# Performance work log

Hardware: AMD Instinct MI355X
Metric: run time of the kernel (lower is better)

The kernel has to match this reference:

```python
import jax, jax.numpy as jnp
import numpy as np

N = 50000      # nodes
E = 800000     # edges (avg degree 16)
IN = 128       # in_dim
OUT = 128      # out_dim
K = 4          # Chebyshev order
NEIG = 64      # num_eigs
H = 128        # eigval_hidden_dim
BN_EPS = 1e-5


def setup_inputs() -> dict:
    key = jax.random.key(0)
    ks = jax.random.split(key, 12)
    feature = jax.random.normal(ks[0], (N, IN), jnp.float32)
    # linear over concat of (K Chebyshev blocks + 1 spectral block) = (K+1)*IN
    lin_w = jax.random.normal(ks[1], ((K + 1) * IN, OUT), jnp.float32) / np.sqrt((K + 1) * IN)
    lin_b = jnp.zeros((OUT,), jnp.float32)
    # eigval_filter MLP: 1 -> H -> H -> 1 (ReLU between)
    ew0 = jax.random.normal(ks[2], (1, H), jnp.float32)
    eb0 = jnp.zeros((H,), jnp.float32)
    ew1 = jax.random.normal(ks[3], (H, H), jnp.float32) / np.sqrt(H)
    eb1 = jnp.zeros((H,), jnp.float32)
    ew2 = jax.random.normal(ks[4], (H, 1), jnp.float32) / np.sqrt(H)
    eb2 = jnp.zeros((1,), jnp.float32)
    bn_gamma = jnp.ones((OUT,), jnp.float32)
    bn_beta = jnp.zeros((OUT,), jnp.float32)
    lambda_max = jnp.ones((1,), jnp.float32)
    # cached (detached) spectral data for the graph
    evecs = jax.random.normal(ks[5], (N, NEIG), jnp.float32)
    evals = jax.random.uniform(ks[6], (NEIG,), jnp.float32)
    edge_src = jax.random.randint(ks[7], (E,), 0, N, jnp.int32).astype(jnp.int64)
    edge_dst = jax.random.randint(ks[8], (E,), 0, N, jnp.int32).astype(jnp.int64)
    return dict(feature=feature, lin_w=lin_w, lin_b=lin_b, ew0=ew0, eb0=eb0,
                ew1=ew1, eb1=eb1, ew2=ew2, eb2=eb2, bn_gamma=bn_gamma,
                bn_beta=bn_beta, lambda_max=lambda_max, evecs=evecs,
                evals=evals, edge_src=edge_src, edge_dst=edge_dst)


def reference(feature, lin_w, lin_b, ew0, eb0, ew1, eb1, ew2, eb2,
              bn_gamma, bn_beta, lambda_max, evecs, evals, edge_src, edge_dst):
    src = edge_src.astype(jnp.int32)
    dst = edge_dst.astype(jnp.int32)
    # in-degrees (messages arrive at dst) and D^-1/2, clamped at 1
    deg = jax.ops.segment_sum(jnp.ones((E,), jnp.float32), dst, num_segments=N)
    d_sqrt = jnp.clip(deg, 1.0, None) ** -0.5  # [N]
    d_sqrt = d_sqrt[:, None]                   # [N,1]

    def unn_laplacian(x):
        m = (x * d_sqrt)[src]                              # [E,IN]
        agg = jax.ops.segment_sum(m, dst, num_segments=N)  # [N,IN]
        return agg * d_sqrt

    re_norm = 2.0 / lambda_max  # broadcast scalar (per-node in dgl, constant here)

    X0 = feature
    blocks = [X0]
    h = unn_laplacian(X0)
    X1 = -re_norm * h + X0 * (re_norm - 1.0)
    blocks.append(X1)
    for _ in range(2, K):
        h = unn_laplacian(X1)
        Xi = -2.0 * re_norm * h + X1 * 2.0 * (re_norm - 1.0) - X0
        blocks.append(Xi)
        X1, X0 = Xi, X1

    # spectral filtering: evecs^T f, scale by MLP(evals), project back
    z = jax.nn.relu(evals[:, None] @ ew0 + eb0)   # [NEIG,H]
    z = jax.nn.relu(z @ ew1 + eb1)                # [NEIG,H]
    ef = z @ ew2 + eb2                            # [NEIG,1]
    hs = jnp.einsum('ne,nf->ef', evecs, feature)  # [NEIG,IN]
    hs = ef * hs
    hs = jnp.einsum('ne,ef->nf', evecs, hs)       # [N,IN]
    blocks.append(hs)

    Xt = jnp.concatenate(blocks, axis=1)          # [N,(K+1)*IN]
    out = Xt @ lin_w + lin_b                      # [N,OUT]

    # BatchNorm1d (training-mode batch statistics, biased variance)
    mu = jnp.mean(out, axis=0)
    var = jnp.mean((out - mu) ** 2, axis=0)
    out = (out - mu) * jax.lax.rsqrt(var + BN_EPS) * bn_gamma + bn_beta
    out = jax.nn.relu(out)
    # dropout p=0.0 -> identity; residual disabled
    return out
```

## Files before the change

### kernel.cpp

```cpp
#include <hip/hip_runtime.h>

#define N_NODES 50000
#define N_EDGES 800000
#define IN_F    128
#define OUT_F   128
#define NEIG    64
#define HDIM    128
#define BN_EPSF 1e-5f
#define XB_ROWS 50048
#define XB_COLS 640
#define SCAN_BLK 49
#define HSP_BLOCKS 521
#define HSP_NODES 96
#define RED_CHUNK 33
#define RED_SPLIT 16

typedef __attribute__((ext_vector_type(8))) short short8;
typedef __attribute__((ext_vector_type(4))) float floatx4;

#define OFF_XB      0
#define OFF_X1F     (XB_ROWS * XB_COLS / 2)
#define OFF_X2F     (OFF_X1F + N_NODES * IN_F)
#define OFF_WT      (OFF_X2F + N_NODES * IN_F)
#define OFF_DSQRT   (OFF_WT + 40960)
#define OFF_HS      (OFF_DSQRT + N_NODES)
#define OFF_EF      (OFF_HS + NEIG * OUT_F)
#define OFF_COLSUM  (OFF_EF + NEIG)
#define OFF_COLSQ   (OFF_COLSUM + OUT_F)
#define OFF_DEG     (OFF_COLSQ + OUT_F)
#define OFF_ROWSTART (OFF_DEG + N_NODES)
#define OFF_CSR     (OFF_ROWSTART + N_NODES + 1)
#define OFF_BSUM    (OFF_CSR + N_EDGES)
#define OFF_RANK    (OFF_BSUM + 64)

static __device__ inline unsigned short f2bf(float f) {
    union { float f; unsigned int u; } v; v.f = f;
    unsigned int r = (v.u + 0x7FFFu + ((v.u >> 16) & 1u)) >> 16;
    return (unsigned short)r;
}
static __device__ inline float bf2f(unsigned int u16) {
    union { unsigned int u; float f; } v; v.u = u16 << 16;
    return v.f;
}

__global__ __launch_bounds__(256) void k_prep(const float* __restrict__ feat,
                                              const float* __restrict__ W,
                                              unsigned short* __restrict__ Xb,
                                              unsigned short* __restrict__ Wt,
                                              int* __restrict__ deg,
                                              float* __restrict__ small) {
    int b = blockIdx.x;
    if (b < 3125) {
        int t = b * 256 + threadIdx.x;
        int n = t >> 4, c8 = (t & 15) * 8;
        float4 a = *(const float4*)&feat[n * IN_F + c8];
        float4 bb = *(const float4*)&feat[n * IN_F + c8 + 4];
        ushort4 o0, o1;
        o0.x = f2bf(a.x); o0.y = f2bf(a.y); o0.z = f2bf(a.z); o0.w = f2bf(a.w);
        o1.x = f2bf(bb.x); o1.y = f2bf(bb.y); o1.z = f2bf(bb.z); o1.w = f2bf(bb.w);
        *(ushort4*)&Xb[(size_t)n * XB_COLS + c8]     = o0;
        *(ushort4*)&Xb[(size_t)n * XB_COLS + c8 + 4] = o1;
    } else if (b < 3445) {
        int t = (b - 3125) * 256 + threadIdx.x;
        int k = t >> 7, n = t & 127;
        Wt[n * 640 + k] = f2bf(W[k * 128 + n]);
    } else {
        int i = (b - 3445) * 256 + threadIdx.x;
        if (i < N_NODES) deg[i] = 0;
        if (i < NEIG * OUT_F + NEIG + 2 * OUT_F) small[i] = 0.0f;
    }
}

__global__ void k_rank(int* __restrict__ deg, const int* __restrict__ dst,
                       int* __restrict__ rank) {
    int e = blockIdx.x * 256 + threadIdx.x;
    if (e < N_EDGES) rank[e] = atomicAdd(&deg[dst[e]], 1);
}

__global__ __launch_bounds__(1024) void k_scan1(const int* __restrict__ deg,
                                                int* __restrict__ row_start,
                                                int* __restrict__ bsum) {
    __shared__ int sd[1024];
    int i = blockIdx.x * 1024 + threadIdx.x;
    int v = (i < N_NODES) ? deg[i] : 0;
    sd[threadIdx.x] = v;
    __syncthreads();
    for (int off = 1; off < 1024; off <<= 1) {
        int t = (threadIdx.x >= off) ? sd[threadIdx.x - off] : 0;
        __syncthreads();
        sd[threadIdx.x] += t;
        __syncthreads();
    }
    if (i < N_NODES) row_start[i] = sd[threadIdx.x] - v;
    if (threadIdx.x == 1023) bsum[blockIdx.x] = sd[1023];
}

__global__ void k_scan2(int* __restrict__ bsum) {
    int t = threadIdx.x;
    int orig = (t < SCAN_BLK) ? bsum[t] : 0;
    int v = orig;
    for (int off = 1; off < 64; off <<= 1) {
        int u = __shfl_up(v, off);
        if (t >= off) v += u;
    }
    if (t < SCAN_BLK) bsum[t] = v - orig;
}

__global__ __launch_bounds__(1024) void k_scan3(const int* __restrict__ deg,
                                                int* __restrict__ row_start,
                                                const int* __restrict__ bsum,
                                                float* __restrict__ dsq) {
    int i = blockIdx.x * 1024 + threadIdx.x;
    if (i < N_NODES) {
        int r = row_start[i] + bsum[blockIdx.x];
        row_start[i] = r;
        dsq[i] = rsqrtf((float)max(deg[i], 1));
    }
    if (i == 0) row_start[N_NODES] = N_EDGES;
}

__global__ void k_csr(const int* __restrict__ src, const int* __restrict__ dst,
                      const int* __restrict__ rank, const int* __restrict__ row_start,
                      int* __restrict__ csr_src) {
    int e = blockIdx.x * 256 + threadIdx.x;
    if (e < N_EDGES) csr_src[row_start[dst[e]] + rank[e]] = src[e];
}

__global__ __launch_bounds__(256) void k_gather(const int* __restrict__ row_start,
                                                const int* __restrict__ csr_src,
                                                const float* __restrict__ dsq,
                                                const unsigned short* __restrict__ srcb,
                                                const unsigned short* __restrict__ prevb,
                                                const unsigned short* __restrict__ ppb,
                                                unsigned short* __restrict__ outb,
                                                const float* __restrict__ lm, int first) {
    int n = (blockIdx.x * 256 + threadIdx.x) >> 6;
    int lane = threadIdx.x & 63;
    if (n >= N_NODES) return;
    float rn = 2.0f / lm[0];
    float ax = 0.0f, ay = 0.0f;
    int beg = row_start[n], end = row_start[n + 1];
    int i = beg;
    for (; i + 16 <= end; i += 16) {
        int s[16]; float c[16]; unsigned int p[16];
#pragma unroll
        for (int j = 0; j < 16; ++j) s[j] = __builtin_amdgcn_readfirstlane(csr_src[i + j]);
#pragma unroll
        for (int j = 0; j < 16; ++j) c[j] = dsq[s[j]];
#pragma unroll
        for (int j = 0; j < 16; ++j)
            p[j] = *(const unsigned int*)&srcb[(size_t)s[j] * XB_COLS + lane * 2];
#pragma unroll
        for (int j = 0; j < 16; ++j) {
            ax += c[j] * bf2f(p[j] & 0xffffu);
            ay += c[j] * bf2f(p[j] >> 16);
        }
    }
    for (; i + 8 <= end; i += 8) {
        int s[8]; float c[8]; unsigned int p[8];
#pragma unroll
        for (int j = 0; j < 8; ++j) s[j] = __builtin_amdgcn_readfirstlane(csr_src[i + j]);
#pragma unroll
        for (int j = 0; j < 8; ++j) c[j] = dsq[s[j]];
#pragma unroll
        for (int j = 0; j < 8; ++j)
            p[j] = *(const unsigned int*)&srcb[(size_t)s[j] * XB_COLS + lane * 2];
#pragma unroll
        for (int j = 0; j < 8; ++j) {
            ax += c[j] * bf2f(p[j] & 0xffffu);
            ay += c[j] * bf2f(p[j] >> 16);
        }
    }
    for (; i + 4 <= end; i += 4) {
        int s[4]; float c[4]; unsigned int p[4];
#pragma unroll
        for (int j = 0; j < 4; ++j) s[j] = __builtin_amdgcn_readfirstlane(csr_src[i + j]);
#pragma unroll
        for (int j = 0; j < 4; ++j) c[j] = dsq[s[j]];
#pragma unroll
        for (int j = 0; j < 4; ++j)
            p[j] = *(const unsigned int*)&srcb[(size_t)s[j] * XB_COLS + lane * 2];
#pragma unroll
        for (int j = 0; j < 4; ++j) {
            ax += c[j] * bf2f(p[j] & 0xffffu);
            ay += c[j] * bf2f(p[j] >> 16);
        }
    }
    for (; i < end; ++i) {
        int s = __builtin_amdgcn_readfirstlane(csr_src[i]);
        float sc = dsq[s];
        unsigned int pv = *(const unsigned int*)&srcb[(size_t)s * XB_COLS + lane * 2];
        ax += sc * bf2f(pv & 0xffffu);
        ay += sc * bf2f(pv >> 16);
    }
    float ds = dsq[n];
    float a = (first ? -rn : -2.0f * rn) * ds;
    float b = first ? (rn - 1.0f) : 2.0f * (rn - 1.0f);
    unsigned int pu = *(const unsigned int*)&prevb[(size_t)n * XB_COLS + lane * 2];
    float rx = a * ax + b * bf2f(pu & 0xffffu);
    float ry = a * ay + b * bf2f(pu >> 16);
    if (ppb) {
        unsigned int qu = *(const unsigned int*)&ppb[(size_t)n * XB_COLS + lane * 2];
        rx -= bf2f(qu & 0xffffu);
        ry -= bf2f(qu >> 16);
    }
    unsigned int packed = (unsigned int)f2bf(rx) | ((unsigned int)f2bf(ry) << 16);
    *(unsigned int*)&outb[(size_t)n * XB_COLS + lane * 2] = packed;
}

__global__ __launch_bounds__(128) void k_ef2(const float* __restrict__ evals,
                                             const float* __restrict__ ew0,
                                             const float* __restrict__ eb0,
                                             const float* __restrict__ ew1,
                                             const float* __restrict__ eb1,
                                             const float* __restrict__ ew2,
                                             const float* __restrict__ eb2,
                                             float* __restrict__ ef) {
    __shared__ float z0[HDIM];
    __shared__ float red[HDIM];
    int i = blockIdx.x, j = threadIdx.x;
    float ev = evals[i];
    z0[j] = fmaxf(0.0f, ev * ew0[j] + eb0[j]);
    __syncthreads();
    float s0 = 0.f, s1 = 0.f, s2 = 0.f, s3 = 0.f;
    for (int h = 0; h < HDIM; h += 4) {
        s0 += z0[h]     * ew1[(h) * HDIM + j];
        s1 += z0[h + 1] * ew1[(h + 1) * HDIM + j];
        s2 += z0[h + 2] * ew1[(h + 2) * HDIM + j];
        s3 += z0[h + 3] * ew1[(h + 3) * HDIM + j];
    }
    float z1 = fmaxf(0.0f, eb1[j] + s0 + s1 + s2 + s3);
    red[j] = z1 * ew2[j];
    __syncthreads();
    for (int off = 64; off > 0; off >>= 1) {
        if (j < off) red[j] += red[j + off];
        __syncthreads();
    }
    if (j == 0) ef[i] = red[0] + eb2[0];
}

__global__ __launch_bounds__(256) void k_hs_partial2(const float* __restrict__ evecs,
                                                     const float* __restrict__ feat,
                                                     float* __restrict__ partials) {
    __shared__ float sEv[32 * NEIG];
    __shared__ float sFt[32 * IN_F];
    int t = threadIdx.x;
    int e0 = (t >> 5) * 8;
    int f0 = (t & 31) * 4;
    float acc[8][4];
#pragma unroll
    for (int r = 0; r < 8; ++r)
#pragma unroll
        for (int c = 0; c < 4; ++c) acc[r][c] = 0.0f;

    int n0 = blockIdx.x * HSP_NODES;
    for (int ch = 0; ch < HSP_NODES; ch += 32) {
        int base = n0 + ch;
        {
            int r = t >> 3, c = (t & 7) * 8;
            int n = base + r;
            float4 a, b;
            if (n < N_NODES) {
                a = *(const float4*)&evecs[(size_t)n * NEIG + c];
                b = *(const float4*)&evecs[(size_t)n * NEIG + c + 4];
            } else {
                a = make_float4(0, 0, 0, 0); b = a;
            }
            *(float4*)&sEv[r * NEIG + c] = a;
            *(float4*)&sEv[r * NEIG + c + 4] = b;
        }
        {
            int r = t >> 3, c = (t & 7) * 16;
            int n = base + r;
#pragma unroll
            for (int q = 0; q < 4; ++q) {
                float4 v = (n < N_NODES) ? *(const float4*)&feat[(size_t)n * IN_F + c + q * 4]
                                         : make_float4(0, 0, 0, 0);
                *(float4*)&sFt[r * IN_F + c + q * 4] = v;
            }
        }
        __syncthreads();
#pragma unroll 2
        for (int i = 0; i < 32; ++i) {
            float4 ev0 = *(float4*)&sEv[i * NEIG + e0];
            float4 ev1 = *(float4*)&sEv[i * NEIG + e0 + 4];
            float4 fv  = *(float4*)&sFt[i * IN_F + f0];
            float evv[8] = {ev0.x, ev0.y, ev0.z, ev0.w, ev1.x, ev1.y, ev1.z, ev1.w};
#pragma unroll
            for (int r = 0; r < 8; ++r) {
                acc[r][0] += evv[r] * fv.x;
                acc[r][1] += evv[r] * fv.y;
                acc[r][2] += evv[r] * fv.z;
                acc[r][3] += evv[r] * fv.w;
            }
        }
        __syncthreads();
    }
    float* p = &partials[(size_t)blockIdx.x * (NEIG * IN_F)];
#pragma unroll
    for (int r = 0; r < 8; ++r)
        *(float4*)&p[(e0 + r) * IN_F + f0] = make_float4(acc[r][0], acc[r][1], acc[r][2], acc[r][3]);
}

__global__ __launch_bounds__(256) void k_hs_reduce(const float* __restrict__ partials,
                                                   float* __restrict__ hs_small) {
    int grp   = blockIdx.x & 31;
    int chunk = blockIdx.x >> 5;
    int idx = grp * 256 + threadIdx.x;
    int j0 = chunk * RED_CHUNK;
    int j1 = min(j0 + RED_CHUNK, HSP_BLOCKS);
    float s = 0.0f;
    for (int j = j0; j < j1; ++j) s += partials[(size_t)j * (NEIG * IN_F) + idx];
    atomicAdd(&hs_small[idx], s);
}

__global__ __launch_bounds__(256) void k_hs_apply2(unsigned short* __restrict__ Xb,
                                                   const float* __restrict__ evecs,
                                                   const float* __restrict__ hs_small,
                                                   const float* __restrict__ ef) {
    __shared__ float sShs[NEIG * HDIM];
    __shared__ float sEv[32 * NEIG];
    int t = threadIdx.x;
    int n0 = blockIdx.x * 32;
    {
        float efv = ef[t >> 2];
        int pbase = t * 32;
#pragma unroll
        for (int q = 0; q < 8; ++q) {
            float4 v = *(const float4*)&hs_small[pbase + q * 4];
            v.x *= efv; v.y *= efv; v.z *= efv; v.w *= efv;
            *(float4*)&sShs[pbase + q * 4] = v;
        }
    }
    {
        int r = t >> 3, c = (t & 7) * 8;
        int n = n0 + r;
        float4 a, b;
        if (n < N_NODES) {
            a = *(const float4*)&evecs[(size_t)n * NEIG + c];
            b = *(const float4*)&evecs[(size_t)n * NEIG + c + 4];
        } else {
            a = make_float4(0, 0, 0, 0); b = a;
        }
        *(float4*)&sEv[r * NEIG + c] = a;
        *(float4*)&sEv[r * NEIG + c + 4] = b;
    }
    __syncthreads();
    int nb = (t >> 5) * 4;
    int f0 = (t & 31) * 4;
    float acc[4][4];
#pragma unroll
    for (int q = 0; q < 4; ++q)
#pragma unroll
        for (int c = 0; c < 4; ++c) acc[q][c] = 0.0f;
    for (int e = 0; e < NEIG; ++e) {
        float4 sv = *(float4*)&sShs[e * HDIM + f0];
#pragma unroll
        for (int q = 0; q < 4; ++q) {
            float evv = sEv[(nb + q) * NEIG + e];
            acc[q][0] += evv * sv.x;
            acc[q][1] += evv * sv.y;
            acc[q][2] += evv * sv.z;
            acc[q][3] += evv * sv.w;
        }
    }
#pragma unroll
    for (int q = 0; q < 4; ++q) {
        int n = n0 + nb + q;
        if (n < N_NODES) {
            ushort4 o;
            o.x = f2bf(acc[q][0]); o.y = f2bf(acc[q][1]);
            o.z = f2bf(acc[q][2]); o.w = f2bf(acc[q][3]);
            *(ushort4*)&Xb[(size_t)n * XB_COLS + 4 * IN_F + f0] = o;
        }
    }
}

__global__ __launch_bounds__(256) void k_gemm(const unsigned short* __restrict__ Xb,
                                              const unsigned short* __restrict__ Wt,
                                              const float* __restrict__ bias,
                                              float* __restrict__ out,
                                              float* __restrict__ colsum,
                                              float* __restrict__ colsq) {
    __shared__ unsigned short sA[128 * 32];
    __shared__ unsigned short sB[128 * 32];
    __shared__ float cs[4][OUT_F];
    __shared__ float cq[4][OUT_F];
    int tid = threadIdx.x;
    int wave = tid >> 6, lane = tid & 63;
    int quad = lane >> 4, m16 = lane & 15;
    int row0 = blockIdx.x * 128;

    floatx4 acc[2][8];
#pragma unroll
    for (int mt = 0; mt < 2; ++mt)
#pragma unroll
        for (int nt = 0; nt < 8; ++nt) acc[mt][nt] = (floatx4)(0.0f);

    int r  = tid >> 2;
    int c8 = (tid & 3) * 8;
    int gr0 = min(row0 + r, N_NODES - 1);
    int gr1 = min(row0 + r + 64, N_NODES - 1);

    for (int k0 = 0; k0 < 640; k0 += 32) {
        *(uint4*)&sA[r * 32 + c8]        = *(const uint4*)&Xb[(size_t)gr0 * XB_COLS + k0 + c8];
        *(uint4*)&sA[(r + 64) * 32 + c8] = *(const uint4*)&Xb[(size_t)gr1 * XB_COLS + k0 + c8];
        *(uint4*)&sB[r * 32 + c8]        = *(const uint4*)&Wt[r * 640 + k0 + c8];
        *(uint4*)&sB[(r + 64) * 32 + c8] = *(const uint4*)&Wt[(r + 64) * 640 + k0 + c8];
        __syncthreads();
        short8 a0 = *(short8*)&sA[(wave * 32 + m16) * 32 + quad * 8];
        short8 a1 = *(short8*)&sA[(wave * 32 + 16 + m16) * 32 + quad * 8];
#pragma unroll
        for (int nt = 0; nt < 8; ++nt) {
            short8 b = *(short8*)&sB[(nt * 16 + m16) * 32 + quad * 8];
            acc[0][nt] = __builtin_amdgcn_mfma_f32_16x16x32_bf16(a0, b, acc[0][nt], 0, 0, 0);
            acc[1][nt] = __builtin_amdgcn_mfma_f32_16x16x32_bf16(a1, b, acc[1][nt], 0, 0, 0);
        }
        __syncthreads();
    }
#pragma unroll
    for (int nt = 0; nt < 8; ++nt) {
        int col = nt * 16 + m16;
        float bb = bias[col];
        float sv = 0.0f, sq = 0.0f;
#pragma unroll
        for (int mt = 0; mt < 2; ++mt) {
            int rbase = row0 + wave * 32 + mt * 16 + quad * 4;
#pragma unroll
            for (int reg = 0; reg < 4; ++reg) {
                int row = rbase + reg;
                if (row < N_NODES) {
                    float w = acc[mt][nt][reg] + bb;
                    out[(size_t)row * OUT_F + col] = w;
                    sv += w;
                    sq += w * w;
                }
            }
        }
        sv += __shfl_down(sv, 32); sq += __shfl_down(sq, 32);
        sv += __shfl_down(sv, 16); sq += __shfl_down(sq, 16);
        if (lane < 16) { cs[wave][col] = sv; cq[wave][col] = sq; }
    }
    __syncthreads();
    if (tid < OUT_F) {
        float s = cs[0][tid] + cs[1][tid] + cs[2][tid] + cs[3][tid];
        float q = cq[0][tid] + cq[1][tid] + cq[2][tid] + cq[3][tid];
        atomicAdd(&colsum[tid], s);
        atomicAdd(&colsq[tid], q);
    }
}

__global__ void k_bn_apply(float* __restrict__ out, const float* __restrict__ colsum,
                           const float* __restrict__ colsq, const float* __restrict__ gamma,
                           const float* __restrict__ beta) {
    int t = blockIdx.x * 256 + threadIdx.x;
    int n = t >> 5, c = t & 31;
    float4 v = *(float4*)&out[n * OUT_F + c * 4];
    float4 s = *(const float4*)&colsum[c * 4];
    float4 q = *(const float4*)&colsq[c * 4];
    float4 g = *(const float4*)&gamma[c * 4];
    float4 b = *(const float4*)&beta[c * 4];
    const float invN = 1.0f / (float)N_NODES;
    float mux = s.x * invN, muy = s.y * invN, muz = s.z * invN, muw = s.w * invN;
    float ix = rsqrtf(q.x * invN - mux * mux + BN_EPSF);
    float iy = rsqrtf(q.y * invN - muy * muy + BN_EPSF);
    float iz = rsqrtf(q.z * invN - muz * muz + BN_EPSF);
    float iw = rsqrtf(q.w * invN - muw * muw + BN_EPSF);
    v.x = fmaxf(0.0f, (v.x - mux) * ix * g.x + b.x);
    v.y = fmaxf(0.0f, (v.y - muy) * iy * g.y + b.y);
    v.z = fmaxf(0.0f, (v.z - muz) * iz * g.z + b.z);
    v.w = fmaxf(0.0f, (v.w - muw) * iw * g.w + b.w);
    *(float4*)&out[n * OUT_F + c * 4] = v;
}

extern "C" void kernel_launch(void* const* d_in, const int* in_sizes, int n_in,
                              void* d_out, int out_size, void* d_ws, size_t ws_size,
                              hipStream_t stream) {
    const float* feature    = (const float*)d_in[0];
    const float* lin_w      = (const float*)d_in[1];
    const float* lin_b      = (const float*)d_in[2];
    const float* ew0        = (const float*)d_in[3];
    const float* eb0        = (const float*)d_in[4];
    const float* ew1        = (const float*)d_in[5];
    const float* eb1        = (const float*)d_in[6];
    const float* ew2        = (const float*)d_in[7];
    const float* eb2        = (const float*)d_in[8];
    const float* bn_gamma   = (const float*)d_in[9];
    const float* bn_beta    = (const float*)d_in[10];
    const float* lambda_max = (const float*)d_in[11];
    const float* evecs      = (const float*)d_in[12];
    const float* evals      = (const float*)d_in[13];
    const int*   edge_src   = (const int*)d_in[14];
    const int*   edge_dst   = (const int*)d_in[15];

    float* out = (float*)d_out;
    float* ws  = (float*)d_ws;
    unsigned short* Xb = (unsigned short*)(ws + OFF_XB);
    unsigned short* Wt = (unsigned short*)(ws + OFF_WT);
    float* dsq      = ws + OFF_DSQRT;
    float* hs_small = ws + OFF_HS;
    float* ef       = ws + OFF_EF;
    float* colsum   = ws + OFF_COLSUM;
    float* colsq   = ws + OFF_COLSQ;
    int*   deg      = (int*)(ws + OFF_DEG);
    int*   row_start= (int*)(ws + OFF_ROWSTART);
    int*   csr_src  = (int*)(ws + OFF_CSR);
    int*   bsum     = (int*)(ws + OFF_BSUM);
    int*   rank     = (int*)(ws + OFF_RANK);
    float* partials = ws + OFF_X1F;

    k_prep<<<3674, 256, 0, stream>>>(feature, lin_w, Xb, Wt, deg, hs_small);
    k_rank<<<(N_EDGES + 255) / 256, 256, 0, stream>>>(deg, edge_dst, rank);
    k_scan1<<<SCAN_BLK, 1024, 0, stream>>>(deg, row_start, bsum);
    k_scan2<<<1, 64, 0, stream>>>(bsum);
    k_scan3<<<SCAN_BLK, 1024, 0, stream>>>(deg, row_start, bsum, dsq);
    k_csr<<<(N_EDGES + 255) / 256, 256, 0, stream>>>(edge_src, edge_dst, rank, row_start, csr_src);

    const int GBLK = (N_NODES * 64 + 255) / 256;
    k_gather<<<GBLK, 256, 0, stream>>>(row_start, csr_src, dsq,
                                       Xb + 0, Xb + 0, (const unsigned short*)nullptr,
                                       Xb + IN_F, lambda_max, 1);
    k_gather<<<GBLK, 256, 0, stream>>>(row_start, csr_src, dsq,
                                       Xb + IN_F, Xb + IN_F, Xb + 0,
                                       Xb + 2 * IN_F, lambda_max, 0);
    k_gather<<<GBLK, 256, 0, stream>>>(row_start, csr_src, dsq,
                                       Xb + 2 * IN_F, Xb + 2 * IN_F, Xb + IN_F,
                                       Xb + 3 * IN_F, lambda_max, 0);

    k_ef2<<<NEIG, 128, 0, stream>>>(evals, ew0, eb0, ew1, eb1, ew2, eb2, ef);
    k_hs_partial2<<<HSP_BLOCKS, 256, 0, stream>>>(evecs, feature, partials);
    k_hs_reduce<<<32 * RED_SPLIT, 256, 0, stream>>>(partials, hs_small);
    k_hs_apply2<<<(N_NODES + 31) / 32, 256, 0, stream>>>(Xb, evecs, hs_small, ef);

    k_gemm<<<(N_NODES + 127) / 128, 256, 0, stream>>>(Xb, Wt, lin_b, out, colsum, colsq);
    k_bn_apply<<<(N_NODES * 32) / 256, 256, 0, stream>>>(out, colsum, colsq, bn_gamma, bn_beta);
}
```

Before: 367.3 us.

## Co-schedule spectral branch with CSR build and replicate degree counters

Merges independent kernels into combined launches by block-index ranges. The spectral partial-GEMM and eigenvalue MLP now share a launch with the edge rank atomics, the hs reduction shares one with the scan, and the spectral apply shares one with the CSR scatter. Degree counters are replicated 8 ways by edge index to cut atomic contention on hot destination nodes, which needs per-replica offsets (rs4) and a wider zero-init. The aim is fewer launches and better device fill for small kernels. In exchange, shared-memory use and register pressure are set by the heaviest branch of each merged kernel, and extra memory traffic is added for the replicas.

```diff
diff --git a/kernel.cpp b/kernel.cpp
--- a/kernel.cpp
+++ b/kernel.cpp
@@ -13,7 +13,7 @@
 #define HSP_BLOCKS 521
 #define HSP_NODES 96
 #define RED_CHUNK 33
-#define RED_SPLIT 16
+#define N_REP 8
 
 typedef __attribute__((ext_vector_type(8))) short short8;
 typedef __attribute__((ext_vector_type(4))) float floatx4;
@@ -28,10 +28,11 @@
 #define OFF_COLSUM  (OFF_EF + NEIG)
 #define OFF_COLSQ   (OFF_COLSUM + OUT_F)
 #define OFF_DEG     (OFF_COLSQ + OUT_F)
-#define OFF_ROWSTART (OFF_DEG + N_NODES)
+#define OFF_ROWSTART (OFF_DEG + N_REP * N_NODES)
 #define OFF_CSR     (OFF_ROWSTART + N_NODES + 1)
 #define OFF_BSUM    (OFF_CSR + N_EDGES)
 #define OFF_RANK    (OFF_BSUM + 64)
+#define OFF_RS4     (OFF_RANK + N_EDGES)
 
 static __device__ inline unsigned short f2bf(float f) {
     union { float f; unsigned int u; } v; v.f = f;
@@ -47,7 +48,7 @@
                                               const float* __restrict__ W,
                                               unsigned short* __restrict__ Xb,
                                               unsigned short* __restrict__ Wt,
-                                              int* __restrict__ deg,
+                                              int* __restrict__ degR,
                                               float* __restrict__ small) {
     int b = blockIdx.x;
     if (b < 3125) {
@@ -66,33 +67,171 @@
         Wt[n * 640 + k] = f2bf(W[k * 128 + n]);
     } else {
         int i = (b - 3445) * 256 + threadIdx.x;
-        if (i < N_NODES) deg[i] = 0;
+        if (i < N_REP * N_NODES) degR[i] = 0;
         if (i < NEIG * OUT_F + NEIG + 2 * OUT_F) small[i] = 0.0f;
     }
 }
 
-__global__ void k_rank(int* __restrict__ deg, const int* __restrict__ dst,
-                       int* __restrict__ rank) {
-    int e = blockIdx.x * 256 + threadIdx.x;
-    if (e < N_EDGES) rank[e] = atomicAdd(&deg[dst[e]], 1);
-}
-
-__global__ __launch_bounds__(1024) void k_scan1(const int* __restrict__ deg,
-                                                int* __restrict__ row_start,
-                                                int* __restrict__ bsum) {
-    __shared__ int sd[1024];
-    int i = blockIdx.x * 1024 + threadIdx.x;
-    int v = (i < N_NODES) ? deg[i] : 0;
-    sd[threadIdx.x] = v;
-    __syncthreads();
-    for (int off = 1; off < 1024; off <<= 1) {
-        int t = (threadIdx.x >= off) ? sd[threadIdx.x - off] : 0;
+__global__ __launch_bounds__(256) void k_stage2(const float* __restrict__ evecs,
+                                                const float* __restrict__ feat,
+                                                float* __restrict__ partials,
+                                                const float* __restrict__ evals,
+                                                const float* __restrict__ ew0,
+                                                const float* __restrict__ eb0,
+                                                const float* __restrict__ ew1,
+                                                const float* __restrict__ eb1,
+                                                const float* __restrict__ ew2,
+                                                const float* __restrict__ eb2,
+                                                float* __restrict__ ef,
+                                                int* __restrict__ degR,
+                                                const int* __restrict__ dst,
+                                                int* __restrict__ rank) {
+    int b = blockIdx.x;
+    int t = threadIdx.x;
+    if (b < HSP_BLOCKS) {
+        __shared__ float sEv[32 * NEIG];
+        __shared__ float sFt[32 * IN_F];
+        int e0 = (t >> 5) * 8;
+        int f0 = (t & 31) * 4;
+        float acc[8][4];
+#pragma unroll
+        for (int r = 0; r < 8; ++r)
+#pragma unroll
+            for (int c = 0; c < 4; ++c) acc[r][c] = 0.0f;
+
+        int n0 = b * HSP_NODES;
+        for (int ch = 0; ch < HSP_NODES; ch += 32) {
+            int base = n0 + ch;
+            {
+                int r = t >> 3, c = (t & 7) * 8;
+                int n = base + r;
+                float4 a, bb;
+                if (n < N_NODES) {
+                    a = *(const float4*)&evecs[(size_t)n * NEIG + c];
+                    bb = *(const float4*)&evecs[(size_t)n * NEIG + c + 4];
+                } else {
+                    a = make_float4(0, 0, 0, 0); bb = a;
+                }
+                *(float4*)&sEv[r * NEIG + c] = a;
+                *(float4*)&sEv[r * NEIG + c + 4] = bb;
+            }
+            {
+                int r = t >> 3, c = (t & 7) * 16;
+                int n = base + r;
+#pragma unroll
+                for (int q = 0; q < 4; ++q) {
+                    float4 v = (n < N_NODES) ? *(const float4*)&feat[(size_t)n * IN_F + c + q * 4]
+                                             : make_float4(0, 0, 0, 0);
+                    *(float4*)&sFt[r * IN_F + c + q * 4] = v;
+                }
+            }
+            __syncthreads();
+#pragma unroll 2
+            for (int i = 0; i < 32; ++i) {
+                float4 ev0 = *(float4*)&sEv[i * NEIG + e0];
+                float4 ev1 = *(float4*)&sEv[i * NEIG + e0 + 4];
+                float4 fv  = *(float4*)&sFt[i * IN_F + f0];
+                float evv[8] = {ev0.x, ev0.y, ev0.z, ev0.w, ev1.x, ev1.y, ev1.z, ev1.w};
+#pragma unroll
+                for (int r = 0; r < 8; ++r) {
+                    acc[r][0] += evv[r] * fv.x;
+                    acc[r][1] += evv[r] * fv.y;
+                    acc[r][2] += evv[r] * fv.z;
+                    acc[r][3] += evv[r] * fv.w;
+                }
+            }
+            __syncthreads();
+        }
+        float* p = &partials[(size_t)b * (NEIG * IN_F)];
+#pragma unroll
+        for (int r = 0; r < 8; ++r)
+            *(float4*)&p[(e0 + r) * IN_F + f0] = make_float4(acc[r][0], acc[r][1], acc[r][2], acc[r][3]);
+    } else if (b < HSP_BLOCKS + 32) {
+        __shared__ float z0[2][HDIM];
+        __shared__ float red[2][HDIM];
+        int sub = t >> 7, j = t & 127;
+        int i = (b - HSP_BLOCKS) * 2 + sub;
+        float ev = evals[i];
+        z0[sub][j] = fmaxf(0.0f, ev * ew0[j] + eb0[j]);
         __syncthreads();
-        sd[threadIdx.x] += t;
+        float s0 = 0.f, s1 = 0.f, s2 = 0.f, s3 = 0.f;
+        for (int h = 0; h < HDIM; h += 4) {
+            s0 += z0[sub][h]     * ew1[(h) * HDIM + j];
+            s1 += z0[sub][h + 1] * ew1[(h + 1) * HDIM + j];
+            s2 += z0[sub][h + 2] * ew1[(h + 2) * HDIM + j];
+            s3 += z0[sub][h + 3] * ew1[(h + 3) * HDIM + j];
+        }
+        float z1 = fmaxf(0.0f, eb1[j] + s0 + s1 + s2 + s3);
+        red[sub][j] = z1 * ew2[j];
         __syncthreads();
-    }
-    if (i < N_NODES) row_start[i] = sd[threadIdx.x] - v;
-    if (threadIdx.x == 1023) bsum[blockIdx.x] = sd[1023];
+        for (int off = 64; off > 0; off >>= 1) {
+            if (j < off) red[sub][j] += red[sub][j + off];
+            __syncthreads();
+        }
+        if (j == 0) ef[i] = red[sub][0] + eb2[0];
+    } else {
+        int e = (b - (HSP_BLOCKS + 32)) * 256 + t;
+        if (e < N_EDGES) {
+            int rep = e & (N_REP - 1);
+            rank[e] = atomicAdd(&degR[rep * N_NODES + dst[e]], 1);
+        }
+    }
+}
+
+__global__ __launch_bounds__(1024) void k_stage3(int* __restrict__ degR,
+                                                 int* __restrict__ row_start,
+                                                 int* __restrict__ bsum,
+                                                 const float* __restrict__ partials,
+                                                 float* __restrict__ hs_small) {
+    int b = blockIdx.x;
+    int t = threadIdx.x;
+    if (b < SCAN_BLK) {
+        __shared__ int sd[1024];
+        int i = b * 1024 + t;
+        int d0 = 0, d1 = 0, d2 = 0, d3 = 0, d4 = 0, d5 = 0, d6 = 0, d7 = 0;
+        if (i < N_NODES) {
+            d0 = degR[i];
+            d1 = degR[N_NODES + i];
+            d2 = degR[2 * N_NODES + i];
+            d3 = degR[3 * N_NODES + i];
+            d4 = degR[4 * N_NODES + i];
+            d5 = degR[5 * N_NODES + i];
+            d6 = degR[6 * N_NODES + i];
+            d7 = degR[7 * N_NODES + i];
+        }
+        int total = d0 + d1 + d2 + d3 + d4 + d5 + d6 + d7;
+        sd[t] = total;
+        __syncthreads();
+        for (int off = 1; off < 1024; off <<= 1) {
+            int v = (t >= off) ? sd[t - off] : 0;
+            __syncthreads();
+            sd[t] += v;
+            __syncthreads();
+        }
+        if (i < N_NODES) {
+            row_start[i] = sd[t] - total;
+            degR[i] = total;
+            int p = d0;
+            degR[N_NODES + i] = p;     p += d1;
+            degR[2 * N_NODES + i] = p; p += d2;
+            degR[3 * N_NODES + i] = p; p += d3;
+            degR[4 * N_NODES + i] = p; p += d4;
+            degR[5 * N_NODES + i] = p; p += d5;
+            degR[6 * N_NODES + i] = p; p += d6;
+            degR[7 * N_NODES + i] = p;
+        }
+        if (t == 1023) bsum[b] = sd[1023];
+    } else {
+        int b2 = b - SCAN_BLK;
+        int grp = b2 & 7;
+        int chunk = b2 >> 3;
+        int idx = grp * 1024 + t;
+        int j0 = chunk * RED_CHUNK;
+        int j1 = min(j0 + RED_CHUNK, HSP_BLOCKS);
+        float s = 0.0f;
+        for (int j = j0; j < j1; ++j) s += partials[(size_t)j * (NEIG * IN_F) + idx];
+        atomicAdd(&hs_small[idx], s);
+    }
 }
 
 __global__ void k_scan2(int* __restrict__ bsum) {
@@ -106,24 +245,98 @@
     if (t < SCAN_BLK) bsum[t] = v - orig;
 }
 
-__global__ __launch_bounds__(1024) void k_scan3(const int* __restrict__ deg,
+__global__ __launch_bounds__(1024) void k_scan3(const int* __restrict__ degR,
                                                 int* __restrict__ row_start,
                                                 const int* __restrict__ bsum,
-                                                float* __restrict__ dsq) {
+                                                float* __restrict__ dsq,
+                                                int* __restrict__ rs4) {
     int i = blockIdx.x * 1024 + threadIdx.x;
     if (i < N_NODES) {
         int r = row_start[i] + bsum[blockIdx.x];
         row_start[i] = r;
-        dsq[i] = rsqrtf((float)max(deg[i], 1));
+        rs4[i] = r;
+#pragma unroll
+        for (int rep = 1; rep < N_REP; ++rep)
+            rs4[rep * N_NODES + i] = r + degR[rep * N_NODES + i];
+        dsq[i] = rsqrtf((float)max(degR[i], 1));
     }
     if (i == 0) row_start[N_NODES] = N_EDGES;
 }
 
-__global__ void k_csr(const int* __restrict__ src, const int* __restrict__ dst,
-                      const int* __restrict__ rank, const int* __restrict__ row_start,
-                      int* __restrict__ csr_src) {
-    int e = blockIdx.x * 256 + threadIdx.x;
-    if (e < N_EDGES) csr_src[row_start[dst[e]] + rank[e]] = src[e];
+__global__ __launch_bounds__(256) void k_stage6(const int* __restrict__ src,
+                                                const int* __restrict__ dst,
+                                                const int* __restrict__ rank,
+                                                const int* __restrict__ rs4,
+                                                int* __restrict__ csr_src,
+                                                unsigned short* __restrict__ Xb,
+                                                const float* __restrict__ evecs,
+                                                const float* __restrict__ hs_small,
+                                                const float* __restrict__ ef) {
+    int b = blockIdx.x;
+    int t = threadIdx.x;
+    if (b < 3125) {
+        int e = b * 256 + t;
+        if (e < N_EDGES) {
+            int rep = e & (N_REP - 1);
+            csr_src[rs4[rep * N_NODES + dst[e]] + rank[e]] = src[e];
+        }
+    } else {
+        __shared__ float sShs[NEIG * HDIM];
+        __shared__ float sEv[32 * NEIG];
+        int n0 = (b - 3125) * 32;
+        {
+            float efv = ef[t >> 2];
+            int pbase = t * 32;
+#pragma unroll
+            for (int q = 0; q < 8; ++q) {
+                float4 v = *(const float4*)&hs_small[pbase + q * 4];
+                v.x *= efv; v.y *= efv; v.z *= efv; v.w *= efv;
+                *(float4*)&sShs[pbase + q * 4] = v;
+            }
+        }
+        {
+            int r = t >> 3, c = (t & 7) * 8;
+            int n = n0 + r;
+            float4 a, bb;
+            if (n < N_NODES) {
+                a = *(const float4*)&evecs[(size_t)n * NEIG + c];
+                bb = *(const float4*)&evecs[(size_t)n * NEIG + c + 4];
+            } else {
+                a = make_float4(0, 0, 0, 0); bb = a;
+            }
+            *(float4*)&sEv[r * NEIG + c] = a;
+            *(float4*)&sEv[r * NEIG + c + 4] = bb;
+        }
+        __syncthreads();
+        int nb = (t >> 5) * 4;
+        int f0 = (t & 31) * 4;
+        float acc[4][4];
+#pragma unroll
+        for (int q = 0; q < 4; ++q)
+#pragma unroll
+            for (int c = 0; c < 4; ++c) acc[q][c] = 0.0f;
+        for (int e = 0; e < NEIG; ++e) {
+            float4 sv = *(float4*)&sShs[e * HDIM + f0];
+#pragma unroll
+            for (int q = 0; q < 4; ++q) {
+                float evv = sEv[(nb + q) * NEIG + e];
+                acc[q][0] += evv * sv.x;
+                acc[q][1] += evv * sv.y;
+                acc[q][2] += evv * sv.z;
+                acc[q][3] += evv * sv.w;
+            }
+        }
+#pragma unroll
+        for (int q = 0; q < 4; ++q) {
+            int n = n0 + nb + q;
+            if (n < N_NODES) {
+                ushort4 o;
+                o.x = f2bf(acc[q][0]); o.y = f2bf(acc[q][1]);
+                o.z = f2bf(acc[q][2]); o.w = f2bf(acc[q][3]);
+                *(ushort4*)&Xb[(size_t)n * XB_COLS + 4 * IN_F + f0] = o;
+            }
+        }
+    }
 }
 
 __global__ __launch_bounds__(256) void k_gather(const int* __restrict__ row_start,
@@ -206,174 +419,6 @@
     }
     unsigned int packed = (unsigned int)f2bf(rx) | ((unsigned int)f2bf(ry) << 16);
     *(unsigned int*)&outb[(size_t)n * XB_COLS + lane * 2] = packed;
-}
-
-__global__ __launch_bounds__(128) void k_ef2(const float* __restrict__ evals,
-                                             const float* __restrict__ ew0,
-                                             const float* __restrict__ eb0,
-                                             const float* __restrict__ ew1,
-                                             const float* __restrict__ eb1,
-                                             const float* __restrict__ ew2,
-                                             const float* __restrict__ eb2,
-                                             float* __restrict__ ef) {
-    __shared__ float z0[HDIM];
-    __shared__ float red[HDIM];
-    int i = blockIdx.x, j = threadIdx.x;
-    float ev = evals[i];
-    z0[j] = fmaxf(0.0f, ev * ew0[j] + eb0[j]);
-    __syncthreads();
-    float s0 = 0.f, s1 = 0.f, s2 = 0.f, s3 = 0.f;
-    for (int h = 0; h < HDIM; h += 4) {
-        s0 += z0[h]     * ew1[(h) * HDIM + j];
-        s1 += z0[h + 1] * ew1[(h + 1) * HDIM + j];
-        s2 += z0[h + 2] * ew1[(h + 2) * HDIM + j];
-        s3 += z0[h + 3] * ew1[(h + 3) * HDIM + j];
-    }
-    float z1 = fmaxf(0.0f, eb1[j] + s0 + s1 + s2 + s3);
-    red[j] = z1 * ew2[j];
-    __syncthreads();
-    for (int off = 64; off > 0; off >>= 1) {
-        if (j < off) red[j] += red[j + off];
-        __syncthreads();
-    }
-    if (j == 0) ef[i] = red[0] + eb2[0];
-}
-
-__global__ __launch_bounds__(256) void k_hs_partial2(const float* __restrict__ evecs,
-                                                     const float* __restrict__ feat,
-                                                     float* __restrict__ partials) {
-    __shared__ float sEv[32 * NEIG];
-    __shared__ float sFt[32 * IN_F];
-    int t = threadIdx.x;
-    int e0 = (t >> 5) * 8;
-    int f0 = (t & 31) * 4;
-    float acc[8][4];
-#pragma unroll
-    for (int r = 0; r < 8; ++r)
-#pragma unroll
-        for (int c = 0; c < 4; ++c) acc[r][c] = 0.0f;
-
-    int n0 = blockIdx.x * HSP_NODES;
-    for (int ch = 0; ch < HSP_NODES; ch += 32) {
-        int base = n0 + ch;
-        {
-            int r = t >> 3, c = (t & 7) * 8;
-            int n = base + r;
-            float4 a, b;
-            if (n < N_NODES) {
-                a = *(const float4*)&evecs[(size_t)n * NEIG + c];
-                b = *(const float4*)&evecs[(size_t)n * NEIG + c + 4];
-            } else {
-                a = make_float4(0, 0, 0, 0); b = a;
-            }
-            *(float4*)&sEv[r * NEIG + c] = a;
-            *(float4*)&sEv[r * NEIG + c + 4] = b;
-        }
-        {
-            int r = t >> 3, c = (t & 7) * 16;
-            int n = base + r;
-#pragma unroll
-            for (int q = 0; q < 4; ++q) {
-                float4 v = (n < N_NODES) ? *(const float4*)&feat[(size_t)n * IN_F + c + q * 4]
-                                         : make_float4(0, 0, 0, 0);
-                *(float4*)&sFt[r * IN_F + c + q * 4] = v;
-            }
-        }
-        __syncthreads();
-#pragma unroll 2
-        for (int i = 0; i < 32; ++i) {
-            float4 ev0 = *(float4*)&sEv[i * NEIG + e0];
-            float4 ev1 = *(float4*)&sEv[i * NEIG + e0 + 4];
-            float4 fv  = *(float4*)&sFt[i * IN_F + f0];
-            float evv[8] = {ev0.x, ev0.y, ev0.z, ev0.w, ev1.x, ev1.y, ev1.z, ev1.w};
-#pragma unroll
-            for (int r = 0; r < 8; ++r) {
-                acc[r][0] += evv[r] * fv.x;
-                acc[r][1] += evv[r] * fv.y;
-                acc[r][2] += evv[r] * fv.z;
-                acc[r][3] += evv[r] * fv.w;
-            }
-        }
-        __syncthreads();
-    }
-    float* p = &partials[(size_t)blockIdx.x * (NEIG * IN_F)];
-#pragma unroll
-    for (int r = 0; r < 8; ++r)
-        *(float4*)&p[(e0 + r) * IN_F + f0] = make_float4(acc[r][0], acc[r][1], acc[r][2], acc[r][3]);
-}
-
-__global__ __launch_bounds__(256) void k_hs_reduce(const float* __restrict__ partials,
-                                                   float* __restrict__ hs_small) {
-    int grp   = blockIdx.x & 31;
-    int chunk = blockIdx.x >> 5;
-    int idx = grp * 256 + threadIdx.x;
-    int j0 = chunk * RED_CHUNK;
-    int j1 = min(j0 + RED_CHUNK, HSP_BLOCKS);
-    float s = 0.0f;
-    for (int j = j0; j < j1; ++j) s += partials[(size_t)j * (NEIG * IN_F) + idx];
-    atomicAdd(&hs_small[idx], s);
-}
-
-__global__ __launch_bounds__(256) void k_hs_apply2(unsigned short* __restrict__ Xb,
-                                                   const float* __restrict__ evecs,
-                                                   const float* __restrict__ hs_small,
-                                                   const float* __restrict__ ef) {
-    __shared__ float sShs[NEIG * HDIM];
-    __shared__ float sEv[32 * NEIG];
-    int t = threadIdx.x;
-    int n0 = blockIdx.x * 32;
-    {
-        float efv = ef[t >> 2];
-        int pbase = t * 32;
-#pragma unroll
-        for (int q = 0; q < 8; ++q) {
-            float4 v = *(const float4*)&hs_small[pbase + q * 4];
-            v.x *= efv; v.y *= efv; v.z *= efv; v.w *= efv;
-            *(float4*)&sShs[pbase + q * 4] = v;
-        }
-    }
-    {
-        int r = t >> 3, c = (t & 7) * 8;
-        int n = n0 + r;
-        float4 a, b;
-        if (n < N_NODES) {
-            a = *(const float4*)&evecs[(size_t)n * NEIG + c];
-            b = *(const float4*)&evecs[(size_t)n * NEIG + c + 4];
-        } else {
-            a = make_float4(0, 0, 0, 0); b = a;
-        }
-        *(float4*)&sEv[r * NEIG + c] = a;
-        *(float4*)&sEv[r * NEIG + c + 4] = b;
-    }
-    __syncthreads();
-    int nb = (t >> 5) * 4;
-    int f0 = (t & 31) * 4;
-    float acc[4][4];
-#pragma unroll
-    for (int q = 0; q < 4; ++q)
-#pragma unroll
-        for (int c = 0; c < 4; ++c) acc[q][c] = 0.0f;
-    for (int e = 0; e < NEIG; ++e) {
-        float4 sv = *(float4*)&sShs[e * HDIM + f0];
-#pragma unroll
-        for (int q = 0; q < 4; ++q) {
-            float evv = sEv[(nb + q) * NEIG + e];
-            acc[q][0] += evv * sv.x;
-            acc[q][1] += evv * sv.y;
-            acc[q][2] += evv * sv.z;
-            acc[q][3] += evv * sv.w;
-        }
-    }
-#pragma unroll
-    for (int q = 0; q < 4; ++q) {
-        int n = n0 + nb + q;
-        if (n < N_NODES) {
-            ushort4 o;
-            o.x = f2bf(acc[q][0]); o.y = f2bf(acc[q][1]);
-            o.z = f2bf(acc[q][2]); o.w = f2bf(acc[q][3]);
-            *(ushort4*)&Xb[(size_t)n * XB_COLS + 4 * IN_F + f0] = o;
-        }
-    }
 }
 
 __global__ __launch_bounds__(256) void k_gemm(const unsigned short* __restrict__ Xb,
@@ -501,20 +546,27 @@
     float* hs_small = ws + OFF_HS;
     float* ef       = ws + OFF_EF;
     float* colsum   = ws + OFF_COLSUM;
-    float* colsq   = ws + OFF_COLSQ;
-    int*   deg      = (int*)(ws + OFF_DEG);
+    float* colsq    = ws + OFF_COLSQ;
+    int*   degR     = (int*)(ws + OFF_DEG);
     int*   row_start= (int*)(ws + OFF_ROWSTART);
     int*   csr_src  = (int*)(ws + OFF_CSR);
     int*   bsum     = (int*)(ws + OFF_BSUM);
     int*   rank     = (int*)(ws + OFF_RANK);
+    int*   rs4      = (int*)(ws + OFF_RS4);
     float* partials = ws + OFF_X1F;
 
-    k_prep<<<3674, 256, 0, stream>>>(feature, lin_w, Xb, Wt, deg, hs_small);
-    k_rank<<<(N_EDGES + 255) / 256, 256, 0, stream>>>(deg, edge_dst, rank);
-    k_scan1<<<SCAN_BLK, 1024, 0, stream>>>(deg, row_start, bsum);
+    k_prep<<<5008, 256, 0, stream>>>(feature, lin_w, Xb, Wt, degR, hs_small);
+
+    k_stage2<<<HSP_BLOCKS + 32 + 3125, 256, 0, stream>>>(evecs, feature, partials,
+                                                         evals, ew0, eb0, ew1, eb1, ew2, eb2,
+                                                         ef, degR, edge_dst, rank);
+
+    k_stage3<<<SCAN_BLK + 128, 1024, 0, stream>>>(degR, row_start, bsum, partials, hs_small);
     k_scan2<<<1, 64, 0, stream>>>(bsum);
-    k_scan3<<<SCAN_BLK, 1024, 0, stream>>>(deg, row_start, bsum, dsq);
-    k_csr<<<(N_EDGES + 255) / 256, 256, 0, stream>>>(edge_src, edge_dst, rank, row_start, csr_src);
+    k_scan3<<<SCAN_BLK, 1024, 0, stream>>>(degR, row_start, bsum, dsq, rs4);
+
+    k_stage6<<<3125 + 1563, 256, 0, stream>>>(edge_src, edge_dst, rank, rs4, csr_src,
+                                              Xb, evecs, hs_small, ef);
 
     const int GBLK = (N_NODES * 64 + 255) / 256;
     k_gather<<<GBLK, 256, 0, stream>>>(row_start, csr_src, dsq,
@@ -527,11 +579,6 @@
                                        Xb + 2 * IN_F, Xb + 2 * IN_F, Xb + IN_F,
                                        Xb + 3 * IN_F, lambda_max, 0);
 
-    k_ef2<<<NEIG, 128, 0, stream>>>(evals, ew0, eb0, ew1, eb1, ew2, eb2, ef);
-    k_hs_partial2<<<HSP_BLOCKS, 256, 0, stream>>>(evecs, feature, partials);
-    k_hs_reduce<<<32 * RED_SPLIT, 256, 0, stream>>>(partials, hs_small);
-    k_hs_apply2<<<(N_NODES + 31) / 32, 256, 0, stream>>>(Xb, evecs, hs_small, ef);
-
     k_gemm<<<(N_NODES + 127) / 128, 256, 0, stream>>>(Xb, Wt, lin_b, out, colsum, colsq);
     k_bn_apply<<<(N_NODES * 32) / 256, 256, 0, stream>>>(out, colsum, colsq, bn_gamma, bn_beta);
 }
```

Result: faster. 342.5 us (-6.7%).
